# Kernel optimization log

Hardware: AMD Instinct MI355X
Metric: run time of the kernel (lower is better)

The kernel has to match this reference:

```python
import jax, jax.numpy as jnp
import numpy as np

VOXEL_SIZE = 0.04


def setup_inputs() -> dict:
    key = jax.random.key(0)
    k1, k2, k3 = jax.random.split(key, 3)
    N, V, C, H, W = 262144, 9, 24, 120, 160
    NVOX = 64
    # sparse voxel coords (N,4): [batch_ind=0, x, y, z]
    xyz = jax.random.randint(k1, (N, 3), 0, NVOX + 1, dtype=jnp.int32)
    coords = jnp.concatenate([jnp.zeros((N, 1), jnp.int32), xyz], axis=1)
    # volume origin chosen so world z is in front of the cameras
    origin = jnp.array([[-1.28, -1.28, 0.5]], dtype=jnp.float32)
    feats = jax.random.normal(k2, (V, C, H, W), dtype=jnp.float32)
    # realistic pinhole projections K @ [I | t_v] (4x4)
    fx = fy = 80.0
    cx, cy = (W - 1) / 2.0, (H - 1) / 2.0
    K = jnp.array([[fx, 0.0, cx], [0.0, fy, cy], [0.0, 0.0, 1.0]], jnp.float32)
    t = jax.random.uniform(k3, (V, 3), minval=-0.1, maxval=0.1, dtype=jnp.float32)
    Rt = jnp.concatenate([jnp.broadcast_to(jnp.eye(3, dtype=jnp.float32), (V, 3, 3)), t[:, :, None]], axis=2)  # (V,3,4)
    P3 = jnp.einsum('ij,vjk->vik', K, Rt)  # (V,3,4)
    last = jnp.broadcast_to(jnp.array([[0.0, 0.0, 0.0, 1.0]], jnp.float32), (V, 1, 4))
    proj = jnp.concatenate([P3, last], axis=1)  # (V,4,4)
    return {"coords": coords, "origin": origin, "feats": feats, "proj": proj}


def _back_project(coords, origin, feats, proj):
    V, C, H, W = feats.shape
    # voxel grid -> world coords
    world = coords[:, 1:].astype(jnp.float32) * VOXEL_SIZE + origin[0]  # (N,3)
    wh = jnp.concatenate([world, jnp.ones_like(world[:, :1])], axis=1)  # (N,4)
    # project into every view
    im_p = jnp.einsum('vij,nj->vni', proj, wh)  # (V,N,4)
    im_x, im_y, im_z = im_p[..., 0], im_p[..., 1], im_p[..., 2]
    px = im_x / im_z  # pixel coords (align_corners=True grid maps back to pixels)
    py = im_y / im_z
    in_bounds = (px >= 0) & (px <= W - 1) & (py >= 0) & (py <= H - 1) & (im_z > 0)  # (V,N)

    # bilinear gather with zero padding
    feats_vhwc = jnp.transpose(feats, (0, 2, 3, 1))  # (V,H,W,C)
    x0 = jnp.floor(px)
    y0 = jnp.floor(py)
    wx1 = px - x0
    wy1 = py - y0
    x0i = x0.astype(jnp.int32)
    y0i = y0.astype(jnp.int32)
    vidx = jnp.arange(V, dtype=jnp.int32)[:, None]

    def corner(xi, yi, w):
        valid = (xi >= 0) & (xi < W) & (yi >= 0) & (yi < H)
        xc = jnp.clip(xi, 0, W - 1)
        yc = jnp.clip(yi, 0, H - 1)
        f = feats_vhwc[vidx, yc, xc]  # (V,N,C) irregular gather
        return f * (w * valid)[..., None]

    samp = (corner(x0i, y0i, (1 - wx1) * (1 - wy1))
            + corner(x0i + 1, y0i, wx1 * (1 - wy1))
            + corner(x0i, y0i + 1, (1 - wx1) * wy1)
            + corner(x0i + 1, y0i + 1, wx1 * wy1))  # (V,N,C)

    samp = samp * in_bounds[..., None]
    z = im_z * in_bounds

    count = jnp.sum(in_bounds.astype(jnp.float32), axis=0)  # (N,)
    valid = count > 0
    denom = jnp.where(valid, count, 1.0)
    vol_feat = jnp.sum(samp, axis=0) / denom[:, None]  # (N,C)

    # normalized mean depth channel
    zsum = jnp.sum(z, axis=0) / denom  # (N,)
    n_valid = jnp.maximum(jnp.sum(valid.astype(jnp.float32)), 1.0)
    zmean = jnp.sum(zsum * valid) / n_valid
    diff = (zsum - zmean) * valid
    zstd = jnp.sqrt(jnp.sum(diff * diff)) + 1e-5  # torch.norm of masked vector
    znorm = jnp.where(valid, (zsum - zmean) / zstd, 0.0)

    volume = jnp.concatenate([vol_feat, znorm[:, None]], axis=1)  # (N,C+1)
    return volume, count


def reference(coords, origin, feats, proj):
    return _back_project(coords, origin, feats, proj)
```

## Files before the change

### kernel.cpp

```cpp
#include <hip/hip_runtime.h>
#include <hip/hip_fp16.h>
#include <math.h>

#define VOXSZ 0.04f
#define NV 9
#define NC 24
#define NH 120
#define NW 160
#define NBINS 262144
#define TBLOCKS (NV * NH)
#define PLANE_BYTES ((size_t)NV * NH * NW * 16)


__device__ __forceinline__ int morton6(int a) {
  a = (a | (a << 8)) & 0x300F;
  a = (a | (a << 4)) & 0x30C3;
  a = (a | (a << 2)) & 0x9249;
  return a;
}

__device__ __forceinline__ int voxel_key(int4 cd) {
  int x = min(max(cd.y, 0), 63), y = min(max(cd.z, 0), 63), z = min(max(cd.w, 0), 63);
  return morton6(x) | (morton6(y) << 1) | (morton6(z) << 2);
}

__global__ __launch_bounds__(256)
void zero_hist_k(int4* __restrict__ hist4) {
  hist4[blockIdx.x * 256 + threadIdx.x] = make_int4(0, 0, 0, 0);
}

__global__ __launch_bounds__(256)
void prep_k(const float* __restrict__ feats, __half* __restrict__ outT,
            const int4* __restrict__ coords, const float* __restrict__ origin,
            const float* __restrict__ proj, int* __restrict__ hist,
            double* __restrict__ partials, float* __restrict__ out, int N) {
  __shared__ __half s[NC][NW + 2];
  __shared__ float s_proj[NV * 12];
  __shared__ float s_org[3];
  __shared__ double s_red[3][4];
  int tid = threadIdx.x;

  if (blockIdx.x < TBLOCKS) {
    int vh = blockIdx.x;
    int v = vh / NH, h = vh % NH;
    const float* ibase = feats + (size_t)v * NC * NH * NW + (size_t)h * NW;
    for (int e = tid; e < NC * (NW / 4); e += 256) {
      int c = e / (NW / 4), w4 = e - c * (NW / 4);
      float4 f = *(const float4*)(ibase + (size_t)c * NH * NW + w4 * 4);
      int w = w4 * 4;
      s[c][w]     = __float2half(f.x);
      s[c][w + 1] = __float2half(f.y);
      s[c][w + 2] = __float2half(f.z);
      s[c][w + 3] = __float2half(f.w);
    }
    __syncthreads();
    for (int j = tid; j < NW * 12; j += 256) {
      int p = j / (NW * 4);
      int rem = j - p * (NW * 4);
      int w = rem >> 2, k = rem & 3;
      __half2 hv = __halves2half2(s[8 * p + 2 * k][w], s[8 * p + 2 * k + 1][w]);
      unsigned int* obase =
          (unsigned int*)((char*)outT + (size_t)p * PLANE_BYTES) + (size_t)vh * NW * 4;
      obase[(w << 2) | k] = *(unsigned int*)&hv;
    }
    return;
  }

  if (tid < NV * 12) s_proj[tid] = proj[(tid / 12) * 16 + (tid % 12)];
  if (tid < 3) s_org[tid] = origin[tid];
  __syncthreads();

  int sid = blockIdx.x - TBLOCKS;
  int n = sid * 256 + tid;
  double rz = 0.0, rz2 = 0.0, rv = 0.0;
  if (n < N) {
    int4 cd = coords[n];
    atomicAdd(&hist[voxel_key(cd)], 1);
    float wx = (float)cd.y * VOXSZ + s_org[0];
    float wy = (float)cd.z * VOXSZ + s_org[1];
    float wz = (float)cd.w * VOXSZ + s_org[2];
    float zs = 0.f; int cnt = 0;
#pragma unroll
    for (int v = 0; v < NV; ++v) {
      const float* P = &s_proj[v * 12];
      float ix = P[0] * wx + P[1] * wy + P[2]  * wz + P[3];
      float iy = P[4] * wx + P[5] * wy + P[6]  * wz + P[7];
      float iz = P[8] * wx + P[9] * wy + P[10] * wz + P[11];
      float px = ix / iz, py = iy / iz;
      bool inb = (px >= 0.f) && (px <= (float)(NW - 1)) &&
                 (py >= 0.f) && (py <= (float)(NH - 1)) && (iz > 0.f);
      if (inb) { cnt++; zs += iz; }
    }
    out[(size_t)N * (NC + 1) + n] = (float)cnt;
    if (cnt > 0) {
      float zsv = zs / (float)cnt;
      rz = (double)zsv; rz2 = (double)zsv * (double)zsv; rv = 1.0;
    }
  }
#pragma unroll
  for (int off = 32; off > 0; off >>= 1) {
    rz  += __shfl_down(rz,  off, 64);
    rz2 += __shfl_down(rz2, off, 64);
    rv  += __shfl_down(rv,  off, 64);
  }
  if ((tid & 63) == 0) {
    int w = tid >> 6;
    s_red[0][w] = rz; s_red[1][w] = rz2; s_red[2][w] = rv;
  }
  __syncthreads();
  if (tid == 0) {
    double a = 0, b = 0, c = 0;
#pragma unroll
    for (int w = 0; w < 4; ++w) { a += s_red[0][w]; b += s_red[1][w]; c += s_red[2][w]; }
    double* p = partials + (size_t)sid * 4;
    p[0] = a; p[1] = b; p[2] = c;
  }
}

__global__ __launch_bounds__(256)
void scanA_k(const int* __restrict__ hist, int* __restrict__ bsum,
             const double* __restrict__ partials, int nblocks,
             float* __restrict__ scal) {
  int tid = threadIdx.x;

  if (blockIdx.x == 256) {
    double rz = 0.0, rz2 = 0.0, rv = 0.0;
    for (int i = tid; i < nblocks; i += 256) {
      const double* p = partials + (size_t)i * 4;
      rz += p[0]; rz2 += p[1]; rv += p[2];
    }
#pragma unroll
    for (int off = 32; off > 0; off >>= 1) {
      rz  += __shfl_down(rz,  off, 64);
      rz2 += __shfl_down(rz2, off, 64);
      rv  += __shfl_down(rv,  off, 64);
    }
    __shared__ double s[3][4];
    if ((tid & 63) == 0) {
      int w = tid >> 6;
      s[0][w] = rz; s[1][w] = rz2; s[2][w] = rv;
    }
    __syncthreads();
    if (tid == 0) {
      double sz = 0, sz2 = 0, nv = 0;
#pragma unroll
      for (int w = 0; w < 4; ++w) { sz += s[0][w]; sz2 += s[1][w]; nv += s[2][w]; }
      double nvm = (nv > 1.0) ? nv : 1.0;
      double zmean = sz / nvm;
      double var = sz2 - 2.0 * zmean * sz + zmean * zmean * nv;
      if (var < 0.0) var = 0.0;
      scal[0] = (float)zmean;
      scal[1] = (float)(sqrt(var) + 1e-5);
    }
    return;
  }

  __shared__ int red[256];
  int4 h = ((const int4*)hist)[blockIdx.x * 256 + tid];
  red[tid] = h.x + h.y + h.z + h.w;
  __syncthreads();
  for (int off = 128; off > 0; off >>= 1) {
    if (tid < off) red[tid] += red[tid + off];
    __syncthreads();
  }
  if (tid == 0) bsum[blockIdx.x] = red[0];
}

__global__ __launch_bounds__(256)
void scanB_k(const int* __restrict__ hist, const int* __restrict__ bsum,
             int* __restrict__ ofs) {
  __shared__ int sb[256];
  __shared__ int st[256];
  int tid = threadIdx.x;

  sb[tid] = bsum[tid];
  __syncthreads();
  for (int off = 1; off < 256; off <<= 1) {
    int v = (tid >= off) ? sb[tid - off] : 0;
    __syncthreads();
    sb[tid] += v;
    __syncthreads();
  }
  int base_blk = (blockIdx.x == 0) ? 0 : sb[blockIdx.x - 1];

  int idx = blockIdx.x * 256 + tid;
  int4 h = ((const int4*)hist)[idx];
  int tsum = h.x + h.y + h.z + h.w;
  st[tid] = tsum;
  __syncthreads();
  for (int off = 1; off < 256; off <<= 1) {
    int v = (tid >= off) ? st[tid - off] : 0;
    __syncthreads();
    st[tid] += v;
    __syncthreads();
  }
  int base = base_blk + st[tid] - tsum;
  int4 o;
  o.x = base;
  o.y = base + h.x;
  o.z = o.y + h.y;
  o.w = o.z + h.z;
  ((int4*)ofs)[idx] = o;
}

__global__ __launch_bounds__(256)
void scatter_k(const int4* __restrict__ coords, int* __restrict__ ofs,
               int2* __restrict__ sorted, int N) {
  int n = blockIdx.x * blockDim.x + threadIdx.x;
  if (n >= N) return;
  int4 cd = coords[n];
  int pos = atomicAdd(&ofs[voxel_key(cd)], 1);
  sorted[pos] = make_int2(cd.y | (cd.z << 7) | (cd.w << 14), n);
}

__global__ __launch_bounds__(192, 4)
void bp_gather_k(const int2* __restrict__ sorted, const float* __restrict__ origin,
                 const float* __restrict__ proj, const __half* __restrict__ featsT,
                 const float* __restrict__ scal, float* __restrict__ out, int N) {
  __shared__ float s_proj[NV * 12];
  __shared__ float s_org[3];
  __shared__ float s_scal[2];
  __shared__ uint2 s_offd[NV][64];
  __shared__ uint2 s_w2[NV][64];
  __shared__ float s_zs[3][64];
  __shared__ int   s_cnt[3][64];
  int tid = threadIdx.x;
  if (tid < NV * 12) s_proj[tid] = proj[(tid / 12) * 16 + (tid % 12)];
  if (tid < 3) s_org[tid] = origin[tid];
  if (tid < 2) s_scal[tid] = scal[tid];
  __syncthreads();

  int nwg = gridDim.x, orig = blockIdx.x;
  int xcd = orig & 7, q = nwg >> 3, r = nwg & 7;
  int bid = (xcd < r ? xcd * (q + 1) : r * (q + 1) + (xcd - r) * q) + (orig >> 3);

  int lane = tid & 63, part = tid >> 6;
  int i = bid * 64 + lane;
  int n = -1, xi = 0, yi = 0, zi = 0;
  if (i < N) {
    int2 rec = sorted[i];
    n = rec.y;
    xi = rec.x & 127; yi = (rec.x >> 7) & 127; zi = (rec.x >> 14) & 127;
  }
  float wx = (float)xi * VOXSZ + s_org[0];
  float wy = (float)yi * VOXSZ + s_org[1];
  float wz = (float)zi * VOXSZ + s_org[2];
  float vm = (n >= 0) ? 1.f : 0.f;

  float zsp = 0.f; int cntp = 0;
#pragma unroll
  for (int qv = 0; qv < 3; ++qv) {
    int v = 3 * part + qv;
    const float* P = &s_proj[v * 12];
    float ix = P[0] * wx + P[1] * wy + P[2]  * wz + P[3];
    float iy = P[4] * wx + P[5] * wy + P[6]  * wz + P[7];
    float iz = P[8] * wx + P[9] * wy + P[10] * wz + P[11];
    float px = ix / iz, py = iy / iz;
    bool inb = (px >= 0.f) && (px <= (float)(NW - 1)) &&
               (py >= 0.f) && (py <= (float)(NH - 1)) && (iz > 0.f);
    float wm = inb ? vm : 0.f;
    cntp += (wm > 0.f) ? 1 : 0;
    zsp = fmaf(wm, iz, zsp);
    float pxc = fminf(fmaxf(px, 0.f), (float)(NW - 1));
    float pyc = fminf(fmaxf(py, 0.f), (float)(NH - 1));
    float x0f = floorf(pxc), y0f = floorf(pyc);
    float fx1 = pxc - x0f, fy1 = pyc - y0f;
    float fx0 = 1.f - fx1, fy0 = 1.f - fy1;
    int x0 = (int)x0f, y0 = (int)y0f;
    unsigned dx = (x0 + 1 < NW) ? 16u : 0u;
    unsigned dy = (y0 + 1 < NH) ? (unsigned)(NW * 16) : 0u;
    unsigned off = (unsigned)(((y0 + v * NH) * NW + x0) * 16);
    __half2 p01 = __halves2half2(__float2half(fx0 * fy0 * wm),
                                 __float2half(fx1 * fy0 * wm));
    __half2 p23 = __halves2half2(__float2half(fx0 * fy1 * wm),
                                 __float2half(fx1 * fy1 * wm));
    s_offd[v][lane] = make_uint2(off, dx | (dy << 16));
    s_w2[v][lane] = make_uint2(*(unsigned int*)&p01, *(unsigned int*)&p23);
  }
  s_zs[part][lane] = zsp;
  s_cnt[part][lane] = cntp;
  __syncthreads();

  int cnt = s_cnt[0][lane] + s_cnt[1][lane] + s_cnt[2][lane];
  __half2 acc2[4];
  const __half2 zero2 = __float2half2_rn(0.f);
#pragma unroll
  for (int c = 0; c < 4; ++c) acc2[c] = zero2;
  const char* fbase = (const char*)featsT + (size_t)part * PLANE_BYTES;

#pragma unroll
  for (int v = 0; v < NV; ++v) {
    uint2 wv = s_w2[v][lane];
    if ((wv.x | wv.y) == 0u) continue;
    uint2 od = s_offd[v][lane];
    unsigned dx = od.y & 0xFFFFu, dy = od.y >> 16;
    const char* p00 = fbase + od.x;
    float4 c00 = *(const float4*)p00;
    float4 c10 = *(const float4*)(p00 + dx);
    float4 c01 = *(const float4*)(p00 + dy);
    float4 c11 = *(const float4*)(p00 + dx + dy);
    __half2 p01 = *(__half2*)&wv.x;
    __half2 p23 = *(__half2*)&wv.y;
    __half2 w00 = __half2half2(__low2half(p01));
    __half2 w10 = __half2half2(__high2half(p01));
    __half2 w01 = __half2half2(__low2half(p23));
    __half2 w11 = __half2half2(__high2half(p23));
    const __half2* h00 = (const __half2*)&c00;
    const __half2* h10 = (const __half2*)&c10;
    const __half2* h01 = (const __half2*)&c01;
    const __half2* h11 = (const __half2*)&c11;
#pragma unroll
    for (int c = 0; c < 4; ++c) acc2[c] = __hfma2(w00, h00[c], acc2[c]);
#pragma unroll
    for (int c = 0; c < 4; ++c) acc2[c] = __hfma2(w10, h10[c], acc2[c]);
#pragma unroll
    for (int c = 0; c < 4; ++c) acc2[c] = __hfma2(w01, h01[c], acc2[c]);
#pragma unroll
    for (int c = 0; c < 4; ++c) acc2[c] = __hfma2(w11, h11[c], acc2[c]);
  }

  if (n < 0) return;
  float denom = (cnt > 0) ? (float)cnt : 1.f;
  float inv = 1.f / denom;
  size_t row = (size_t)n * (NC + 1) + part * 8;
#pragma unroll
  for (int c = 0; c < 4; ++c) {
    float2 t = __half22float2(acc2[c]);
    out[row + 2 * c]     = t.x * inv;
    out[row + 2 * c + 1] = t.y * inv;
  }
  if (part == 2) {
    float zs = s_zs[0][lane] + s_zs[1][lane] + s_zs[2][lane];
    float zsv = zs * inv;
    out[(size_t)n * (NC + 1) + NC] = (cnt > 0) ? (zsv - s_scal[0]) / s_scal[1] : 0.f;
  }
}

__global__ __launch_bounds__(256)
void stats_k(const int4* __restrict__ coords, const float* __restrict__ origin,
             const float* __restrict__ proj, double* __restrict__ partials, int N) {
  __shared__ float s_proj[NV * 12];
  __shared__ float s_org[3];
  __shared__ double s_red[3][4];
  int tid = threadIdx.x;
  if (tid < NV * 12) s_proj[tid] = proj[(tid / 12) * 16 + (tid % 12)];
  if (tid < 3) s_org[tid] = origin[tid];
  __syncthreads();
  int n = blockIdx.x * blockDim.x + tid;
  double rz = 0.0, rz2 = 0.0, rv = 0.0;
  if (n < N) {
    int4 cd = coords[n];
    float wx = (float)cd.y * VOXSZ + s_org[0];
    float wy = (float)cd.z * VOXSZ + s_org[1];
    float wz = (float)cd.w * VOXSZ + s_org[2];
    float zs = 0.f; int cnt = 0;
#pragma unroll
    for (int v = 0; v < NV; ++v) {
      const float* P = &s_proj[v * 12];
      float ix = P[0] * wx + P[1] * wy + P[2]  * wz + P[3];
      float iy = P[4] * wx + P[5] * wy + P[6]  * wz + P[7];
      float iz = P[8] * wx + P[9] * wy + P[10] * wz + P[11];
      float px = ix / iz, py = iy / iz;
      bool inb = (px >= 0.f) && (px <= (float)(NW - 1)) &&
                 (py >= 0.f) && (py <= (float)(NH - 1)) && (iz > 0.f);
      if (inb) { cnt++; zs += iz; }
    }
    if (cnt > 0) {
      float zsv = zs / (float)cnt;
      rz = (double)zsv; rz2 = (double)zsv * (double)zsv; rv = 1.0;
    }
  }
#pragma unroll
  for (int off = 32; off > 0; off >>= 1) {
    rz  += __shfl_down(rz,  off, 64);
    rz2 += __shfl_down(rz2, off, 64);
    rv  += __shfl_down(rv,  off, 64);
  }
  if ((tid & 63) == 0) {
    int w = tid >> 6;
    s_red[0][w] = rz; s_red[1][w] = rz2; s_red[2][w] = rv;
  }
  __syncthreads();
  if (tid == 0) {
    double a = 0, b = 0, c = 0;
#pragma unroll
    for (int w = 0; w < 4; ++w) { a += s_red[0][w]; b += s_red[1][w]; c += s_red[2][w]; }
    double* p = partials + (size_t)blockIdx.x * 4;
    p[0] = a; p[1] = b; p[2] = c;
  }
}

__global__ __launch_bounds__(1024)
void reduce_finalize_k(const double* __restrict__ partials, int nblocks,
                       float* __restrict__ scal) {
  int tid = threadIdx.x;
  double rz = 0.0, rz2 = 0.0, rv = 0.0;
  for (int i = tid; i < nblocks; i += 1024) {
    const double* p = partials + (size_t)i * 4;
    rz += p[0]; rz2 += p[1]; rv += p[2];
  }
#pragma unroll
  for (int off = 32; off > 0; off >>= 1) {
    rz  += __shfl_down(rz,  off, 64);
    rz2 += __shfl_down(rz2, off, 64);
    rv  += __shfl_down(rv,  off, 64);
  }
  __shared__ double s[3][16];
  if ((tid & 63) == 0) {
    int w = tid >> 6;
    s[0][w] = rz; s[1][w] = rz2; s[2][w] = rv;
  }
  __syncthreads();
  if (tid == 0) {
    double sz = 0, sz2 = 0, nv = 0;
#pragma unroll
    for (int w = 0; w < 16; ++w) { sz += s[0][w]; sz2 += s[1][w]; nv += s[2][w]; }
    double nvm = (nv > 1.0) ? nv : 1.0;
    double zmean = sz / nvm;
    double var = sz2 - 2.0 * zmean * sz + zmean * zmean * nv;
    if (var < 0.0) var = 0.0;
    scal[0] = (float)zmean;
    scal[1] = (float)(sqrt(var) + 1e-5);
  }
}

__global__ __launch_bounds__(256)
void bp_fallback_k(const int4* __restrict__ coords, const float* __restrict__ origin,
                   const float* __restrict__ proj, const float* __restrict__ feats,
                   const float* __restrict__ scal, float* __restrict__ out, int N) {
  __shared__ float s_proj[NV * 12];
  __shared__ float s_org[3];
  __shared__ float s_scal[2];
  int tid = threadIdx.x;
  if (tid < NV * 12) s_proj[tid] = proj[(tid / 12) * 16 + (tid % 12)];
  if (tid < 3) s_org[tid] = origin[tid];
  if (tid < 2) s_scal[tid] = scal[tid];
  __syncthreads();
  int n = blockIdx.x * blockDim.x + tid;
  if (n >= N) return;
  int4 cd = coords[n];
  float wx = (float)cd.y * VOXSZ + s_org[0];
  float wy = (float)cd.z * VOXSZ + s_org[1];
  float wz = (float)cd.w * VOXSZ + s_org[2];
  float acc[NC];
#pragma unroll
  for (int c = 0; c < NC; ++c) acc[c] = 0.f;
  float zs = 0.f; int cnt = 0;
#pragma unroll
  for (int v = 0; v < NV; ++v) {
    const float* P = &s_proj[v * 12];
    float ix = P[0] * wx + P[1] * wy + P[2]  * wz + P[3];
    float iy = P[4] * wx + P[5] * wy + P[6]  * wz + P[7];
    float iz = P[8] * wx + P[9] * wy + P[10] * wz + P[11];
    float px = ix / iz, py = iy / iz;
    bool inb = (px >= 0.f) && (px <= (float)(NW - 1)) &&
               (py >= 0.f) && (py <= (float)(NH - 1)) && (iz > 0.f);
    if (!inb) continue;
    cnt++; zs += iz;
    float x0f = floorf(px), y0f = floorf(py);
    float fx1 = px - x0f, fy1 = py - y0f;
    float fx0 = 1.f - fx1, fy0 = 1.f - fy1;
    int x0 = (int)x0f, y0 = (int)y0f;
    int x1 = (x0 + 1 < NW) ? x0 + 1 : NW - 1;
    int y1 = (y0 + 1 < NH) ? y0 + 1 : NH - 1;
    float w00 = fx0 * fy0, w10 = fx1 * fy0, w01 = fx0 * fy1, w11 = fx1 * fy1;
    const float* base = feats + (size_t)v * NC * NH * NW;
#pragma unroll
    for (int c = 0; c < NC; ++c) {
      const float* pc = base + (size_t)c * NH * NW;
      acc[c] += pc[y0 * NW + x0] * w00 + pc[y0 * NW + x1] * w10 +
                pc[y1 * NW + x0] * w01 + pc[y1 * NW + x1] * w11;
    }
  }
  float denom = (cnt > 0) ? (float)cnt : 1.f;
  float inv = 1.f / denom;
  size_t row = (size_t)n * (NC + 1);
#pragma unroll
  for (int c = 0; c < NC; ++c) out[row + c] = acc[c] * inv;
  float zsv = zs * inv;
  out[row + NC] = (cnt > 0) ? (zsv - s_scal[0]) / s_scal[1] : 0.f;
  out[(size_t)N * (NC + 1) + n] = (float)cnt;
}

extern "C" void kernel_launch(void* const* d_in, const int* in_sizes, int n_in,
                              void* d_out, int out_size, void* d_ws, size_t ws_size,
                              hipStream_t stream) {
  const int4*  coords = (const int4*)d_in[0];
  const float* origin = (const float*)d_in[1];
  const float* feats  = (const float*)d_in[2];
  const float* proj   = (const float*)d_in[3];
  float* out = (float*)d_out;
  int N = in_sizes[0] / 4;

  int blocksAll = (N + 255) / 256;

  char* ws = (char*)d_ws;
  float*  scal     = (float*)ws;
  double* partials = (double*)(ws + 64);
  size_t off = 64 + (size_t)blocksAll * 4 * sizeof(double);
  off = (off + 63) & ~(size_t)63;
  __half* featsT = (__half*)(ws + off);
  off += 3 * PLANE_BYTES;
  int* hist = (int*)(ws + off); off += (size_t)NBINS * sizeof(int);
  int* ofs  = (int*)(ws + off); off += (size_t)NBINS * sizeof(int);
  int* bsum = (int*)(ws + off); off += 256 * sizeof(int);
  off = (off + 15) & ~(size_t)15;
  int2* sorted = (int2*)(ws + off); off += (size_t)N * sizeof(int2);
  bool full = (ws_size >= off);

  if (full) {
    zero_hist_k<<<NBINS / 1024, 256, 0, stream>>>((int4*)hist);
    prep_k<<<TBLOCKS + blocksAll, 256, 0, stream>>>(feats, featsT, coords, origin,
                                                    proj, hist, partials, out, N);
    scanA_k<<<257, 256, 0, stream>>>(hist, bsum, partials, blocksAll, scal);
    scanB_k<<<256, 256, 0, stream>>>(hist, bsum, ofs);
    scatter_k<<<blocksAll, 256, 0, stream>>>(coords, ofs, sorted, N);
    int gblocks = (N + 63) / 64;
    bp_gather_k<<<gblocks, 192, 0, stream>>>(sorted, origin, proj, featsT, scal, out, N);
  } else {
    stats_k<<<blocksAll, 256, 0, stream>>>(coords, origin, proj, partials, N);
    reduce_finalize_k<<<1, 1024, 0, stream>>>(partials, blocksAll, scal);
    bp_fallback_k<<<blocksAll, 256, 0, stream>>>(coords, origin, proj, feats, scal, out, N);
  }
}
```

Before: 82.49 us.

## Fuse two-pass histogram scan into single-pass decoupled scan with ticket ordering

Replaces the two scan kernels (block sums, then prefix and offsets) with one kernel that takes block indices from an atomic ticket, publishes each block sum with a flag, and spin-waits on the earlier flags to build its base offset. This removes one kernel launch and the reread of the histogram. It also packs the per-view offset and weight shared-memory arrays into a single uint4 array, so the gather loop does one LDS read per view instead of two. The spin-wait relies on ticket ordering for forward progress, and the flags and ticket are zeroed in the histogram clear kernel.

Result: slower. 85.03 us (+3.1%).

```diff
diff --git a/kernel.cpp b/kernel.cpp
--- a/kernel.cpp
+++ b/kernel.cpp
@@ -10,6 +10,7 @@
 #define NBINS 262144
 #define TBLOCKS (NV * NH)
 #define PLANE_BYTES ((size_t)NV * NH * NW * 16)
+#define SCAN_FLAG 0x40000000
 
 
 __device__ __forceinline__ int morton6(int a) {
@@ -25,8 +26,9 @@
 }
 
 __global__ __launch_bounds__(256)
-void zero_hist_k(int4* __restrict__ hist4) {
+void zero_hist_k(int4* __restrict__ hist4, int4* __restrict__ flags4) {
   hist4[blockIdx.x * 256 + threadIdx.x] = make_int4(0, 0, 0, 0);
+  if (blockIdx.x == 0 && threadIdx.x < 65) flags4[threadIdx.x] = make_int4(0, 0, 0, 0);
 }
 
 __global__ __launch_bounds__(256)
@@ -118,12 +120,18 @@
 }
 
 __global__ __launch_bounds__(256)
-void scanA_k(const int* __restrict__ hist, int* __restrict__ bsum,
-             const double* __restrict__ partials, int nblocks,
-             float* __restrict__ scal) {
+void scan_fused_k(const int* __restrict__ hist, int* __restrict__ flags,
+                  int* __restrict__ ticket, const double* __restrict__ partials,
+                  int nblocks, float* __restrict__ scal, int* __restrict__ ofs) {
+  __shared__ int s_t;
+  __shared__ int red[256];
+  __shared__ int st[256];
   int tid = threadIdx.x;
-
-  if (blockIdx.x == 256) {
+  if (tid == 0) s_t = atomicAdd(ticket, 1);
+  __syncthreads();
+  int t = s_t;
+
+  if (t == 256) {
     double rz = 0.0, rz2 = 0.0, rv = 0.0;
     for (int i = tid; i < nblocks; i += 256) {
       const double* p = partials + (size_t)i * 4;
@@ -155,37 +163,32 @@
     return;
   }
 
-  __shared__ int red[256];
-  int4 h = ((const int4*)hist)[blockIdx.x * 256 + tid];
-  red[tid] = h.x + h.y + h.z + h.w;
+  int4 h = ((const int4*)hist)[t * 256 + tid];
+  int tsum = h.x + h.y + h.z + h.w;
+  red[tid] = tsum;
   __syncthreads();
   for (int off = 128; off > 0; off >>= 1) {
     if (tid < off) red[tid] += red[tid + off];
     __syncthreads();
   }
-  if (tid == 0) bsum[blockIdx.x] = red[0];
-}
-
-__global__ __launch_bounds__(256)
-void scanB_k(const int* __restrict__ hist, const int* __restrict__ bsum,
-             int* __restrict__ ofs) {
-  __shared__ int sb[256];
-  __shared__ int st[256];
-  int tid = threadIdx.x;
-
-  sb[tid] = bsum[tid];
-  __syncthreads();
-  for (int off = 1; off < 256; off <<= 1) {
-    int v = (tid >= off) ? sb[tid - off] : 0;
+  if (tid == 0) atomicExch(&flags[t], SCAN_FLAG | red[0]);
+
+  int myv = 0;
+  if (tid < t) {
+    int f;
+    do { f = atomicOr(&flags[tid], 0); } while (!(f & SCAN_FLAG));
+    myv = f & (SCAN_FLAG - 1);
+  }
+  __syncthreads();
+  red[tid] = myv;
+  __syncthreads();
+  for (int off = 128; off > 0; off >>= 1) {
+    if (tid < off) red[tid] += red[tid + off];
     __syncthreads();
-    sb[tid] += v;
-    __syncthreads();
-  }
-  int base_blk = (blockIdx.x == 0) ? 0 : sb[blockIdx.x - 1];
-
-  int idx = blockIdx.x * 256 + tid;
-  int4 h = ((const int4*)hist)[idx];
-  int tsum = h.x + h.y + h.z + h.w;
+  }
+  int base_blk = red[0];
+  __syncthreads();
+
   st[tid] = tsum;
   __syncthreads();
   for (int off = 1; off < 256; off <<= 1) {
@@ -200,7 +203,7 @@
   o.y = base + h.x;
   o.z = o.y + h.y;
   o.w = o.z + h.z;
-  ((int4*)ofs)[idx] = o;
+  ((int4*)ofs)[t * 256 + tid] = o;
 }
 
 __global__ __launch_bounds__(256)
@@ -220,8 +223,7 @@
   __shared__ float s_proj[NV * 12];
   __shared__ float s_org[3];
   __shared__ float s_scal[2];
-  __shared__ uint2 s_offd[NV][64];
-  __shared__ uint2 s_w2[NV][64];
+  __shared__ uint4 s_pack[NV][64];
   __shared__ float s_zs[3][64];
   __shared__ int   s_cnt[3][64];
   int tid = threadIdx.x;
@@ -274,8 +276,12 @@
                                  __float2half(fx1 * fy0 * wm));
     __half2 p23 = __halves2half2(__float2half(fx0 * fy1 * wm),
                                  __float2half(fx1 * fy1 * wm));
-    s_offd[v][lane] = make_uint2(off, dx | (dy << 16));
-    s_w2[v][lane] = make_uint2(*(unsigned int*)&p01, *(unsigned int*)&p23);
+    uint4 pk;
+    pk.x = off;
+    pk.y = dx | (dy << 16);
+    pk.z = *(unsigned int*)&p01;
+    pk.w = *(unsigned int*)&p23;
+    s_pack[v][lane] = pk;
   }
   s_zs[part][lane] = zsp;
   s_cnt[part][lane] = cntp;
@@ -290,17 +296,16 @@
 
 #pragma unroll
   for (int v = 0; v < NV; ++v) {
-    uint2 wv = s_w2[v][lane];
-    if ((wv.x | wv.y) == 0u) continue;
-    uint2 od = s_offd[v][lane];
-    unsigned dx = od.y & 0xFFFFu, dy = od.y >> 16;
-    const char* p00 = fbase + od.x;
+    uint4 pk = s_pack[v][lane];
+    if ((pk.z | pk.w) == 0u) continue;
+    unsigned dx = pk.y & 0xFFFFu, dy = pk.y >> 16;
+    const char* p00 = fbase + pk.x;
     float4 c00 = *(const float4*)p00;
     float4 c10 = *(const float4*)(p00 + dx);
     float4 c01 = *(const float4*)(p00 + dy);
     float4 c11 = *(const float4*)(p00 + dx + dy);
-    __half2 p01 = *(__half2*)&wv.x;
-    __half2 p23 = *(__half2*)&wv.y;
+    __half2 p01 = *(__half2*)&pk.z;
+    __half2 p23 = *(__half2*)&pk.w;
     __half2 w00 = __half2half2(__low2half(p01));
     __half2 w10 = __half2half2(__high2half(p01));
     __half2 w01 = __half2half2(__low2half(p23));
@@ -503,17 +508,18 @@
   off += 3 * PLANE_BYTES;
   int* hist = (int*)(ws + off); off += (size_t)NBINS * sizeof(int);
   int* ofs  = (int*)(ws + off); off += (size_t)NBINS * sizeof(int);
-  int* bsum = (int*)(ws + off); off += 256 * sizeof(int);
+  int* flags = (int*)(ws + off); off += 260 * sizeof(int);
+  int* ticket = flags + 256;
   off = (off + 15) & ~(size_t)15;
   int2* sorted = (int2*)(ws + off); off += (size_t)N * sizeof(int2);
   bool full = (ws_size >= off);
 
   if (full) {
-    zero_hist_k<<<NBINS / 1024, 256, 0, stream>>>((int4*)hist);
+    zero_hist_k<<<NBINS / 1024, 256, 0, stream>>>((int4*)hist, (int4*)flags);
     prep_k<<<TBLOCKS + blocksAll, 256, 0, stream>>>(feats, featsT, coords, origin,
                                                     proj, hist, partials, out, N);
-    scanA_k<<<257, 256, 0, stream>>>(hist, bsum, partials, blocksAll, scal);
-    scanB_k<<<256, 256, 0, stream>>>(hist, bsum, ofs);
+    scan_fused_k<<<257, 256, 0, stream>>>(hist, flags, ticket, partials,
+                                          blocksAll, scal, ofs);
     scatter_k<<<blocksAll, 256, 0, stream>>>(coords, ofs, sorted, N);
     int gblocks = (N + 63) / 64;
     bp_gather_k<<<gblocks, 192, 0, stream>>>(sorted, origin, proj, featsT, scal, out, N);
```
